# Kernel tuning notes

Measured on AMD Instinct MI355X. Metric: run time of the kernel, lower is better.

The kernel has to match this reference:

```python
import jax, jax.numpy as jnp
import numpy as np

N = 100000   # nodes
E = 1600000  # edges
D = 128      # in_dim == hidden_dim (residual-friendly)
C = 47       # num_classes
EPS = 1e-5   # BatchNorm eps


def _glorot(key, shape):
    fan = shape[0] + shape[1]
    return jax.random.uniform(key, shape, jnp.float32, -1.0, 1.0) * np.sqrt(6.0 / fan)


def setup_inputs() -> dict:
    key = jax.random.key(0)
    ks = jax.random.split(key, 16)
    inp = {
        "x": jax.random.normal(ks[0], (N, D), jnp.float32),
        "edge_index": jax.random.randint(ks[1], (2, E), 0, N, jnp.int32),
    }
    # Per-layer SAGEConv params: lin_l (root, with bias) and lin_r (neighbor, no bias)
    for i, k in zip((1, 2, 3), (ks[2], ks[3], ks[4])):
        k1, k2 = jax.random.split(k)
        inp[f"Wl{i}"] = _glorot(k1, (D, D))
        inp[f"bl{i}"] = jnp.zeros((D,), jnp.float32)
        inp[f"Wr{i}"] = _glorot(k2, (D, D))
        inp[f"bn_g{i}"] = jnp.ones((D,), jnp.float32)
        inp[f"bn_b{i}"] = jnp.zeros((D,), jnp.float32)
    inp["lin_W"] = _glorot(ks[5], (C, D))
    inp["lin_b"] = jnp.zeros((C,), jnp.float32)
    return inp


def _sage_conv(x, src, dst, Wl, bl, Wr):
    # mean aggregation of source features at destination nodes
    msg = jax.ops.segment_sum(x[src], dst, num_segments=N)            # [N, D]
    cnt = jax.ops.segment_sum(jnp.ones((src.shape[0],), x.dtype), dst, num_segments=N)
    mean = msg / jnp.maximum(cnt, 1.0)[:, None]
    return x @ Wl.T + bl + mean @ Wr.T


def _batch_norm(h, g, b):
    mu = h.mean(axis=0)
    var = h.var(axis=0)
    return (h - mu) * jax.lax.rsqrt(var + EPS) * g + b


def reference(x, edge_index,
              Wl1, bl1, Wr1, bn_g1, bn_b1,
              Wl2, bl2, Wr2, bn_g2, bn_b2,
              Wl3, bl3, Wr3, bn_g3, bn_b3,
              lin_W, lin_b):
    src, dst = edge_index[0], edge_index[1]
    layers = [(Wl1, bl1, Wr1, bn_g1, bn_b1),
              (Wl2, bl2, Wr2, bn_g2, bn_b2),
              (Wl3, bl3, Wr3, bn_g3, bn_b3)]
    for Wl, bl, Wr, g, b in layers:
        h = _sage_conv(x, src, dst, Wl, bl, Wr)
        h = jax.nn.relu(_batch_norm(h, g, b))
        # dropout is identity in deterministic/eval reference
        x = x + h  # shapes always match since in_dim == hidden_dim
    return x @ lin_W.T + lin_b
```

## Files before the change

kernel.cpp:

```cpp
#include <hip/hip_runtime.h>

typedef __attribute__((ext_vector_type(8))) short short8;
typedef __attribute__((ext_vector_type(4))) float f32x4;
typedef __attribute__((ext_vector_type(2))) float f32x2;

constexpr int NN = 100000;
constexpr int EE = 1600000;
constexpr int DD = 128;
constexpr int CC = 47;
constexpr int NB = 391;
constexpr int BSLOT = 5120;
constexpr int GB = 782;

constexpr size_t OFF_XB   = 0;
constexpr size_t OFF_MB   = 25600000;
constexpr size_t OFF_HB   = 51200000;
constexpr size_t OFF_XQ   = 76800000;
constexpr size_t OFF_BIN  = 89600000;
constexpr size_t OFF_CSR  = 97607680;
constexpr size_t OFF_RP   = 104007680;
constexpr size_t OFF_CUR  = 104407808;
constexpr size_t OFF_BASE = 104409856;
constexpr size_t OFF_W    = 104411904;
constexpr size_t OFF_ST   = 104620800;

static __device__ __forceinline__ float bf2f(unsigned short u) {
    return __uint_as_float(((unsigned)u) << 16);
}
static __device__ __forceinline__ unsigned short f2bf(float f) {
    unsigned u = __float_as_uint(f);
    unsigned r = (u + 0x7fffu + ((u >> 16) & 1u)) >> 16;
    return (unsigned short)r;
}
static __device__ __forceinline__ uint2 pack8_fp8(const float* f) {
    int w0 = 0, w1 = 0;
    w0 = __builtin_amdgcn_cvt_pk_fp8_f32(f[0], f[1], w0, false);
    w0 = __builtin_amdgcn_cvt_pk_fp8_f32(f[2], f[3], w0, true);
    w1 = __builtin_amdgcn_cvt_pk_fp8_f32(f[4], f[5], w1, false);
    w1 = __builtin_amdgcn_cvt_pk_fp8_f32(f[6], f[7], w1, true);
    return uint2{(unsigned)w0, (unsigned)w1};
}

__global__ void k_prep(const float* __restrict__ wl1, const float* __restrict__ wr1,
                       const float* __restrict__ wl2, const float* __restrict__ wr2,
                       const float* __restrict__ wl3, const float* __restrict__ wr3,
                       const float* __restrict__ lw, unsigned short* __restrict__ wdst,
                       const float* __restrict__ x, unsigned short* __restrict__ xb,
                       unsigned char* __restrict__ xq, int* __restrict__ cur) {
    int bid = blockIdx.x;
    int id = bid * 256 + threadIdx.x;
    if (id < NB) cur[id] = 0;
    if (bid < 408) {
        if (id < 98304) {
            int L = id >> 15;
            int r = id & 32767;
            int mat = r >> 14;
            int t = r & 16383;
            int j = t & 7, lane = (t >> 3) & 63, ct = (t >> 9) & 7, ks = t >> 12;
            int row = ct * 16 + (lane & 15);
            int col = ks * 32 + ((lane >> 4) << 3) + j;
            const float* src = (L == 0) ? (mat ? wr1 : wl1)
                             : (L == 1) ? (mat ? wr2 : wl2)
                                        : (mat ? wr3 : wl3);
            wdst[id] = f2bf(src[row * 128 + col]);
        } else if (id < 98304 + 6144) {
            int t = id - 98304;
            int j = t & 7, lane = (t >> 3) & 63, m = t >> 9;
            int ct = m % 3, ks = m / 3;
            int row = ct * 16 + (lane & 15);
            int col = ks * 32 + ((lane >> 4) << 3) + j;
            wdst[id] = (row < CC) ? f2bf(lw[row * 128 + col]) : (unsigned short)0;
        }
    } else {
        int i = ((bid - 408) * 256 + threadIdx.x) * 8;
        if (i >= NN * DD) return;
        float4 v1 = *(const float4*)(x + i);
        float4 v2 = *(const float4*)(x + i + 4);
        float f[8] = {v1.x, v1.y, v1.z, v1.w, v2.x, v2.y, v2.z, v2.w};
        short8 o;
        #pragma unroll
        for (int j = 0; j < 8; ++j) o[j] = (short)f2bf(f[j]);
        *(short8*)(xb + i) = o;
        *(uint2*)(xq + i) = pack8_fp8(f);
    }
}

__global__ __launch_bounds__(256) void k_bin(const int* __restrict__ ei,
                                             int* __restrict__ cur, int* __restrict__ bin) {
    __shared__ int cnt[NB];
    int t = threadIdx.x;
    for (int b = t; b < NB; b += 256) cnt[b] = 0;
    __syncthreads();
    int start = blockIdx.x * 3125;
    for (int i = t; i < 3125; i += 256) {
        int d = ei[EE + start + i];
        atomicAdd(&cnt[d >> 8], 1);
    }
    __syncthreads();
    int c[2], b0[2];
    #pragma unroll
    for (int k = 0; k < 2; ++k) {
        int b = t + k * 256;
        if (b < NB) { c[k] = cnt[b]; b0[k] = (c[k] > 0) ? atomicAdd(&cur[b], c[k]) : 0; }
    }
    __syncthreads();
    #pragma unroll
    for (int k = 0; k < 2; ++k) {
        int b = t + k * 256;
        if (b < NB) cnt[b] = b0[k];
    }
    __syncthreads();
    for (int i = t; i < 3125; i += 256) {
        int s = ei[start + i];
        int d = ei[EE + start + i];
        int b = d >> 8;
        int p = atomicAdd(&cnt[b], 1);
        if (p < BSLOT) bin[b * BSLOT + p] = (s << 8) | (d & 255);
    }
}

__global__ __launch_bounds__(256) void k_build(const int* __restrict__ cur,
                                               int* __restrict__ rp, const int* __restrict__ bin,
                                               int* __restrict__ csr) {
    __shared__ int lcnt[256], lsc[256], lrun[256], red[256];
    int b = blockIdx.x, t = threadIdx.x;
    int partial = 0;
    for (int i = t; i < b; i += 256) partial += cur[i];
    red[t] = partial;
    __syncthreads();
    for (int off = 128; off > 0; off >>= 1) {
        if (t < off) red[t] += red[t + off];
        __syncthreads();
    }
    int bb = red[0];
    __syncthreads();
    if (b == NB - 1 && t == 0) rp[NN] = bb + cur[b];

    int n0 = b << 8;
    int nodes = NN - n0; if (nodes > 256) nodes = 256;
    int tot = cur[b]; if (tot > BSLOT) tot = BSLOT;
    lcnt[t] = 0;
    __syncthreads();
    const int* bsrc = bin + b * BSLOT;
    for (int i = t; i < tot; i += 256) atomicAdd(&lcnt[bsrc[i] & 255], 1);
    __syncthreads();
    int c = lcnt[t];
    lsc[t] = c;
    __syncthreads();
    for (int off = 1; off < 256; off <<= 1) {
        int v = (t >= off) ? lsc[t - off] : 0;
        __syncthreads();
        lsc[t] += v;
        __syncthreads();
    }
    int excl = lsc[t] - c;
    if (t < nodes) rp[n0 + t] = bb + excl;
    lrun[t] = bb + excl;
    __syncthreads();
    for (int i = t; i < tot; i += 256) {
        int v = bsrc[i];
        int p = atomicAdd(&lrun[v & 255], 1);
        csr[p] = (v >> 8) << 7;
    }
}

__global__ __launch_bounds__(256) void k_agg(const int* __restrict__ rp, const int* __restrict__ csr,
                                             const unsigned char* __restrict__ xq,
                                             unsigned short* __restrict__ mb,
                                             float* __restrict__ st) {
    if (blockIdx.x == 0) st[threadIdx.x] = 0.f;
    int node = blockIdx.x * 4 + (threadIdx.x >> 6);
    if (node >= NN) return;
    int lane = threadIdx.x & 63;
    int g = lane >> 4;
    int cb = (lane & 15) << 3;
    int s0 = rp[node], s1 = rp[node + 1];
    int deg = s1 - s0;
    f32x2 acc0 = {0.f, 0.f}, acc1 = {0.f, 0.f}, acc2 = {0.f, 0.f}, acc3 = {0.f, 0.f};
    int nb = deg >> 4;
    int e = s0 + g;
    for (int k = 0; k < nb; ++k) {
        int i0 = csr[e];
        int i1 = csr[e + 4];
        int i2 = csr[e + 8];
        int i3 = csr[e + 12];
        uint2 v0 = *(const uint2*)(xq + i0 + cb);
        uint2 v1 = *(const uint2*)(xq + i1 + cb);
        uint2 v2 = *(const uint2*)(xq + i2 + cb);
        uint2 v3 = *(const uint2*)(xq + i3 + cb);
        acc0 += __builtin_amdgcn_cvt_pk_f32_fp8(v0.x, false);
        acc1 += __builtin_amdgcn_cvt_pk_f32_fp8(v0.x, true);
        acc2 += __builtin_amdgcn_cvt_pk_f32_fp8(v0.y, false);
        acc3 += __builtin_amdgcn_cvt_pk_f32_fp8(v0.y, true);
        acc0 += __builtin_amdgcn_cvt_pk_f32_fp8(v1.x, false);
        acc1 += __builtin_amdgcn_cvt_pk_f32_fp8(v1.x, true);
        acc2 += __builtin_amdgcn_cvt_pk_f32_fp8(v1.y, false);
        acc3 += __builtin_amdgcn_cvt_pk_f32_fp8(v1.y, true);
        acc0 += __builtin_amdgcn_cvt_pk_f32_fp8(v2.x, false);
        acc1 += __builtin_amdgcn_cvt_pk_f32_fp8(v2.x, true);
        acc2 += __builtin_amdgcn_cvt_pk_f32_fp8(v2.y, false);
        acc3 += __builtin_amdgcn_cvt_pk_f32_fp8(v2.y, true);
        acc0 += __builtin_amdgcn_cvt_pk_f32_fp8(v3.x, false);
        acc1 += __builtin_amdgcn_cvt_pk_f32_fp8(v3.x, true);
        acc2 += __builtin_amdgcn_cvt_pk_f32_fp8(v3.y, false);
        acc3 += __builtin_amdgcn_cvt_pk_f32_fp8(v3.y, true);
        e += 16;
    }
    for (; e < s1; e += 4) {
        int i0 = csr[e];
        uint2 v0 = *(const uint2*)(xq + i0 + cb);
        acc0 += __builtin_amdgcn_cvt_pk_f32_fp8(v0.x, false);
        acc1 += __builtin_amdgcn_cvt_pk_f32_fp8(v0.x, true);
        acc2 += __builtin_amdgcn_cvt_pk_f32_fp8(v0.y, false);
        acc3 += __builtin_amdgcn_cvt_pk_f32_fp8(v0.y, true);
    }
    float acc[8] = {acc0[0], acc0[1], acc1[0], acc1[1],
                    acc2[0], acc2[1], acc3[0], acc3[1]};
    #pragma unroll
    for (int j = 0; j < 8; ++j) {
        acc[j] += __shfl_xor(acc[j], 16);
        acc[j] += __shfl_xor(acc[j], 32);
    }
    if (g == 0) {
        float inv = 1.0f / (float)(deg > 1 ? deg : 1);
        short8 o;
        #pragma unroll
        for (int j = 0; j < 8; ++j) o[j] = (short)f2bf(acc[j] * inv);
        *(short8*)(mb + (size_t)node * 128 + cb) = o;
    }
}

__global__ __launch_bounds__(256, 4) void k_gemm(const unsigned short* __restrict__ xb,
                                                 const unsigned short* __restrict__ mb,
                                                 const unsigned short* __restrict__ wf,
                                                 const float* __restrict__ bias,
                                                 unsigned short* __restrict__ hb,
                                                 float* __restrict__ st) {
    __shared__ unsigned short wsh[16384];
    __shared__ float rbuf[1024];
    int tid = threadIdx.x;
    int wave = tid >> 6, lane = tid & 63, q = lane >> 4, l15 = lane & 15;
    int rowbase = blockIdx.x * 128 + wave * 32;

    f32x4 acc[2][8];
    #pragma unroll
    for (int ct = 0; ct < 8; ++ct) {
        float bv = bias[ct * 16 + l15];
        f32x4 t = {bv, bv, bv, bv};
        acc[0][ct] = t; acc[1][ct] = t;
    }

    #pragma unroll
    for (int mat = 0; mat < 2; ++mat) {
        const unsigned short* src = mat ? mb : xb;
        const int4* wsrc = (const int4*)(wf + (mat << 14));
        if (mat) __syncthreads();
        #pragma unroll
        for (int i = 0; i < 8; ++i)
            ((int4*)wsh)[tid + i * 256] = wsrc[tid + i * 256];
        __syncthreads();
        #pragma unroll
        for (int ks = 0; ks < 4; ++ks) {
            short8 a[2];
            #pragma unroll
            for (int rt = 0; rt < 2; ++rt) {
                int row = rowbase + rt * 16 + l15;
                if (row < NN) a[rt] = *(const short8*)(src + (size_t)row * 128 + ks * 32 + (q << 3));
                else          a[rt] = short8{0,0,0,0,0,0,0,0};
            }
            #pragma unroll
            for (int ct = 0; ct < 8; ++ct) {
                short8 b = *(const short8*)(wsh + ((ks * 8 + ct) << 9) + (lane << 3));
                acc[0][ct] = __builtin_amdgcn_mfma_f32_16x16x32_bf16(a[0], b, acc[0][ct], 0, 0, 0);
                acc[1][ct] = __builtin_amdgcn_mfma_f32_16x16x32_bf16(a[1], b, acc[1][ct], 0, 0, 0);
            }
        }
    }

    #pragma unroll
    for (int ct = 0; ct < 8; ++ct) {
        int colg = ct * 16 + l15;
        float sv = 0.f, qv = 0.f;
        #pragma unroll
        for (int rt = 0; rt < 2; ++rt) {
            #pragma unroll
            for (int r = 0; r < 4; ++r) {
                int row = rowbase + rt * 16 + (q << 2) + r;
                if (row < NN) {
                    float v = acc[rt][ct][r];
                    hb[(size_t)row * 128 + colg] = f2bf(v);
                    sv += v; qv += v * v;
                }
            }
        }
        sv += __shfl_xor(sv, 16); sv += __shfl_xor(sv, 32);
        qv += __shfl_xor(qv, 16); qv += __shfl_xor(qv, 32);
        if (q == 0) {
            rbuf[wave * 256 + colg] = sv;
            rbuf[wave * 256 + 128 + colg] = qv;
        }
    }
    __syncthreads();
    if (tid < 256) {
        float v = rbuf[tid] + rbuf[256 + tid] + rbuf[512 + tid] + rbuf[768 + tid];
        atomicAdd(&st[tid], v);
    }
}

__global__ void k_bn(const unsigned short* __restrict__ hb,
                     const float* __restrict__ stats, const float* __restrict__ gam,
                     const float* __restrict__ bet, unsigned short* __restrict__ xb,
                     unsigned char* __restrict__ xq) {
    int i = (blockIdx.x * 256 + threadIdx.x) * 8;
    if (i >= NN * DD) return;
    int col = i & 127;
    const float invN = 1.0f / (float)NN;
    short8 hv = *(const short8*)(hb + i);
    short8 xv = *(const short8*)(xb + i);
    short8 o;
    float f[8];
    #pragma unroll
    for (int j = 0; j < 8; ++j) {
        int c = col + j;
        float mu = stats[c] * invN;
        float var = stats[128 + c] * invN - mu * mu;
        float sc = rsqrtf(var + 1e-5f) * gam[c];
        float val = (bf2f((unsigned short)hv[j]) - mu) * sc + bet[c];
        float r = bf2f((unsigned short)xv[j]) + (val > 0.f ? val : 0.f);
        f[j] = r;
        o[j] = (short)f2bf(r);
    }
    *(short8*)(xb + i) = o;
    *(uint2*)(xq + i) = pack8_fp8(f);
}

__global__ __launch_bounds__(256) void k_final(const unsigned short* __restrict__ xb,
                                               const unsigned short* __restrict__ wf,
                                               const float* __restrict__ bias,
                                               float* __restrict__ out) {
    __shared__ unsigned short wsh[6144];
    int tid = threadIdx.x;
    #pragma unroll
    for (int i = 0; i < 3; ++i) {
        int idx = tid + i * 256;
        if (idx < 768) ((int4*)wsh)[idx] = ((const int4*)wf)[idx];
    }
    __syncthreads();

    int wave = tid >> 6, lane = tid & 63, q = lane >> 4, l15 = lane & 15;
    int rowbase = blockIdx.x * 256 + wave * 64;

    f32x4 acc[4][3];
    #pragma unroll
    for (int ct = 0; ct < 3; ++ct) {
        int colg = ct * 16 + l15;
        float bv = (colg < CC) ? bias[colg] : 0.f;
        f32x4 t = {bv, bv, bv, bv};
        #pragma unroll
        for (int rt = 0; rt < 4; ++rt) acc[rt][ct] = t;
    }
    #pragma unroll
    for (int ks = 0; ks < 4; ++ks) {
        short8 a[4];
        #pragma unroll
        for (int rt = 0; rt < 4; ++rt) {
            int row = rowbase + rt * 16 + l15;
            if (row < NN) a[rt] = *(const short8*)(xb + (size_t)row * 128 + ks * 32 + (q << 3));
            else          a[rt] = short8{0,0,0,0,0,0,0,0};
        }
        #pragma unroll
        for (int ct = 0; ct < 3; ++ct) {
            short8 b = *(const short8*)(wsh + ((ks * 3 + ct) << 9) + (lane << 3));
            #pragma unroll
            for (int rt = 0; rt < 4; ++rt)
                acc[rt][ct] = __builtin_amdgcn_mfma_f32_16x16x32_bf16(a[rt], b, acc[rt][ct], 0, 0, 0);
        }
    }
    #pragma unroll
    for (int ct = 0; ct < 3; ++ct) {
        int colg = ct * 16 + l15;
        if (colg >= CC) continue;
        #pragma unroll
        for (int rt = 0; rt < 4; ++rt) {
            #pragma unroll
            for (int r = 0; r < 4; ++r) {
                int row = rowbase + rt * 16 + (q << 2) + r;
                if (row < NN) out[(size_t)row * CC + colg] = acc[rt][ct][r];
            }
        }
    }
}

extern "C" void kernel_launch(void* const* d_in, const int* in_sizes, int n_in,
                              void* d_out, int out_size, void* d_ws, size_t ws_size,
                              hipStream_t stream) {
    const float* x   = (const float*)d_in[0];
    const int*   ei  = (const int*)d_in[1];
    const float* Wl[3]  = {(const float*)d_in[2],  (const float*)d_in[7],  (const float*)d_in[12]};
    const float* bl[3]  = {(const float*)d_in[3],  (const float*)d_in[8],  (const float*)d_in[13]};
    const float* Wr[3]  = {(const float*)d_in[4],  (const float*)d_in[9],  (const float*)d_in[14]};
    const float* bng[3] = {(const float*)d_in[5],  (const float*)d_in[10], (const float*)d_in[15]};
    const float* bnb[3] = {(const float*)d_in[6],  (const float*)d_in[11], (const float*)d_in[16]};
    const float* linW = (const float*)d_in[17];
    const float* linb = (const float*)d_in[18];

    char* ws = (char*)d_ws;
    unsigned short* xb   = (unsigned short*)(ws + OFF_XB);
    unsigned short* mb   = (unsigned short*)(ws + OFF_MB);
    unsigned short* hb   = (unsigned short*)(ws + OFF_HB);
    unsigned char*  xq   = (unsigned char*)(ws + OFF_XQ);
    int*            bin  = (int*)(ws + OFF_BIN);
    int*            csr  = (int*)(ws + OFF_CSR);
    int*            rp   = (int*)(ws + OFF_RP);
    int*            cur  = (int*)(ws + OFF_CUR);
    unsigned short* wfr  = (unsigned short*)(ws + OFF_W);
    float*          st   = (float*)(ws + OFF_ST);

    k_prep<<<6658, 256, 0, stream>>>(Wl[0], Wr[0], Wl[1], Wr[1], Wl[2], Wr[2], linW, wfr,
                                     x, xb, xq, cur);
    k_bin<<<512, 256, 0, stream>>>(ei, cur, bin);
    k_build<<<NB, 256, 0, stream>>>(cur, rp, bin, csr);

    for (int l = 0; l < 3; ++l) {
        const unsigned short* wfp = wfr + (size_t)l * 32768;
        k_agg<<<25000, 256, 0, stream>>>(rp, csr, xq, mb, st);
        k_gemm<<<GB, 256, 0, stream>>>(xb, mb, wfp, bl[l], hb, st);
        k_bn<<<6250, 256, 0, stream>>>(hb, st, bng[l], bnb[l], xb, xq);
    }
    k_final<<<391, 256, 0, stream>>>(xb, wfr + 98304, linb, (float*)d_out);
}
```

Measured before the change: 484.4 us.

## Shrink GEMM tile to 64 rows and read weights directly from global

```diff
diff --git a/kernel.cpp b/kernel.cpp
--- a/kernel.cpp
+++ b/kernel.cpp
@@ -10,7 +10,7 @@
 constexpr int CC = 47;
 constexpr int NB = 391;
 constexpr int BSLOT = 5120;
-constexpr int GB = 782;
+constexpr int GB = 1563;
 
 constexpr size_t OFF_XB   = 0;
 constexpr size_t OFF_MB   = 25600000;
@@ -20,7 +20,6 @@
 constexpr size_t OFF_CSR  = 97607680;
 constexpr size_t OFF_RP   = 104007680;
 constexpr size_t OFF_CUR  = 104407808;
-constexpr size_t OFF_BASE = 104409856;
 constexpr size_t OFF_W    = 104411904;
 constexpr size_t OFF_ST   = 104620800;
 
@@ -230,50 +229,46 @@
     }
 }
 
-__global__ __launch_bounds__(256, 4) void k_gemm(const unsigned short* __restrict__ xb,
+__global__ __launch_bounds__(256, 8) void k_gemm(const unsigned short* __restrict__ xb,
                                                  const unsigned short* __restrict__ mb,
                                                  const unsigned short* __restrict__ wf,
                                                  const float* __restrict__ bias,
                                                  unsigned short* __restrict__ hb,
                                                  float* __restrict__ st) {
-    __shared__ unsigned short wsh[16384];
     __shared__ float rbuf[1024];
     int tid = threadIdx.x;
     int wave = tid >> 6, lane = tid & 63, q = lane >> 4, l15 = lane & 15;
-    int rowbase = blockIdx.x * 128 + wave * 32;
-
-    f32x4 acc[2][8];
+    int rowbase = blockIdx.x * 64 + wave * 16;
+    int arow = rowbase + l15;
+
+    f32x4 acc[8];
     #pragma unroll
     for (int ct = 0; ct < 8; ++ct) {
         float bv = bias[ct * 16 + l15];
         f32x4 t = {bv, bv, bv, bv};
-        acc[0][ct] = t; acc[1][ct] = t;
-    }
-
-    #pragma unroll
-    for (int mat = 0; mat < 2; ++mat) {
-        const unsigned short* src = mat ? mb : xb;
-        const int4* wsrc = (const int4*)(wf + (mat << 14));
-        if (mat) __syncthreads();
-        #pragma unroll
-        for (int i = 0; i < 8; ++i)
-            ((int4*)wsh)[tid + i * 256] = wsrc[tid + i * 256];
-        __syncthreads();
-        #pragma unroll
-        for (int ks = 0; ks < 4; ++ks) {
-            short8 a[2];
-            #pragma unroll
-            for (int rt = 0; rt < 2; ++rt) {
-                int row = rowbase + rt * 16 + l15;
-                if (row < NN) a[rt] = *(const short8*)(src + (size_t)row * 128 + ks * 32 + (q << 3));
-                else          a[rt] = short8{0,0,0,0,0,0,0,0};
-            }
-            #pragma unroll
-            for (int ct = 0; ct < 8; ++ct) {
-                short8 b = *(const short8*)(wsh + ((ks * 8 + ct) << 9) + (lane << 3));
-                acc[0][ct] = __builtin_amdgcn_mfma_f32_16x16x32_bf16(a[0], b, acc[0][ct], 0, 0, 0);
-                acc[1][ct] = __builtin_amdgcn_mfma_f32_16x16x32_bf16(a[1], b, acc[1][ct], 0, 0, 0);
-            }
+        acc[ct] = t;
+    }
+
+    #pragma unroll
+    for (int ks = 0; ks < 4; ++ks) {
+        short8 a;
+        if (arow < NN) a = *(const short8*)(xb + (size_t)arow * 128 + ks * 32 + (q << 3));
+        else           a = short8{0,0,0,0,0,0,0,0};
+        #pragma unroll
+        for (int ct = 0; ct < 8; ++ct) {
+            short8 b = *(const short8*)(wf + ((ks * 8 + ct) << 9) + (lane << 3));
+            acc[ct] = __builtin_amdgcn_mfma_f32_16x16x32_bf16(a, b, acc[ct], 0, 0, 0);
+        }
+    }
+    #pragma unroll
+    for (int ks = 0; ks < 4; ++ks) {
+        short8 a;
+        if (arow < NN) a = *(const short8*)(mb + (size_t)arow * 128 + ks * 32 + (q << 3));
+        else           a = short8{0,0,0,0,0,0,0,0};
+        #pragma unroll
+        for (int ct = 0; ct < 8; ++ct) {
+            short8 b = *(const short8*)(wf + 16384 + ((ks * 8 + ct) << 9) + (lane << 3));
+            acc[ct] = __builtin_amdgcn_mfma_f32_16x16x32_bf16(a, b, acc[ct], 0, 0, 0);
         }
     }
 
@@ -282,15 +277,12 @@
         int colg = ct * 16 + l15;
         float sv = 0.f, qv = 0.f;
         #pragma unroll
-        for (int rt = 0; rt < 2; ++rt) {
-            #pragma unroll
-            for (int r = 0; r < 4; ++r) {
-                int row = rowbase + rt * 16 + (q << 2) + r;
-                if (row < NN) {
-                    float v = acc[rt][ct][r];
-                    hb[(size_t)row * 128 + colg] = f2bf(v);
-                    sv += v; qv += v * v;
-                }
+        for (int r = 0; r < 4; ++r) {
+            int row = rowbase + (q << 2) + r;
+            if (row < NN) {
+                float v = acc[ct][r];
+                hb[(size_t)row * 128 + colg] = f2bf(v);
+                sv += v; qv += v * v;
             }
         }
         sv += __shfl_xor(sv, 16); sv += __shfl_xor(sv, 32);
```

Result: slower. 572.1 us (+18.1%).
